# Optimization experiments

Measured on AMD Instinct MI355X. Metric: run time of the kernel, lower is better.

## Reference

```python
import jax, jax.numpy as jnp
import numpy as np

N_E = 1024
E_DIM = 64
BETA = 0.25


def setup_inputs() -> dict:
    key = jax.random.key(0)
    k_z, k_c = jax.random.split(key)
    z = jax.random.normal(k_z, (64, E_DIM, 32, 32), dtype=jnp.float32)  # [B, e_dim, H, W]
    # Codebook initialized uniform(-1/n_e, 1/n_e) as in the torch module
    codebook = jax.random.uniform(k_c, (N_E, E_DIM), dtype=jnp.float32,
                                  minval=-1.0 / N_E, maxval=1.0 / N_E)
    return {"z": z, "codebook": codebook}


def reference(z, codebook):
    beta = BETA
    n_e, e_dim = codebook.shape
    # [B, e_dim, H, W] -> [B, H, W, e_dim]
    z_nhwc = jnp.transpose(z, (0, 2, 3, 1))
    zf = z_nhwc.reshape(-1, e_dim)  # [N, e_dim]
    # Squared Euclidean distances: ||z||^2 + ||e||^2 - 2 z.e  -> [N, n_e]
    d = (jnp.sum(zf * zf, axis=1, keepdims=True)
         + jnp.sum(codebook * codebook, axis=1)
         - 2.0 * jnp.matmul(zf, codebook.T))
    min_encoding_indices = jnp.argmin(d, axis=1)[:, None]  # [N, 1]
    min_encodings = jax.nn.one_hot(min_encoding_indices[:, 0], n_e, dtype=zf.dtype)  # [N, n_e]
    # Gather codebook rows via one-hot matmul (same math as torch version)
    z_q = jnp.matmul(min_encodings, codebook).reshape(z_nhwc.shape)  # [B,H,W,e_dim]
    sg = jax.lax.stop_gradient
    loss = (jnp.mean((sg(z_nhwc) - z_q) ** 2)
            + beta * jnp.mean((z_nhwc - sg(z_q)) ** 2))
    # Straight-through estimator
    z_q = z_nhwc + sg(z_q - z_nhwc)
    z_q = jnp.transpose(z_q, (0, 3, 1, 2))  # back to [B, e_dim, H, W]
    return (loss, z_q, min_encodings, min_encoding_indices)
```

## Files before the change

### kernel.cpp

```cpp
#include <hip/hip_runtime.h>

#define N_ROWS 65536
#define NE 1024
#define ED 64
#define ERR_GAP 8e-5f

static const size_t OFF_ZQ = 1;
static const size_t OFF_ME = 1 + 4194304;
static const size_t OFF_IDX = OFF_ME + (size_t)N_ROWS * NE;
#define ME_FLOATS ((size_t)N_ROWS * NE)

#define SC_CBF  0
#define SC_Z2   65536
#define SC_FLAG 131072

typedef __attribute__((ext_vector_type(8))) short short8v;
typedef __attribute__((ext_vector_type(4))) float f32x4;

__device__ __forceinline__ unsigned bf16_rne(float v) {
  unsigned u = __float_as_uint(v);
  return (u + 0x7FFFu + ((u >> 16) & 1u)) >> 16;
}

__device__ __forceinline__ void gld16(const void* g, void* l) {
  __builtin_amdgcn_global_load_lds(
      (const __attribute__((address_space(1))) void*)g,
      (__attribute__((address_space(3))) void*)l, 16, 0, 0);
}

__global__ __launch_bounds__(256) void k_fill(float* __restrict__ me) {
  const size_t n4 = (ME_FLOATS - 3) >> 2;
  float4* __restrict__ p4 = reinterpret_cast<float4*>(me + 3);
  const size_t stride = (size_t)gridDim.x * blockDim.x;
  const float4 zero4 = make_float4(0.f, 0.f, 0.f, 0.f);
  for (size_t i = blockIdx.x * (size_t)blockDim.x + threadIdx.x; i < n4; i += stride)
    p4[i] = zero4;
  if (blockIdx.x == 0 && threadIdx.x == 0) {
    me[0] = 0.f; me[1] = 0.f; me[2] = 0.f;
    me[ME_FLOATS - 1] = 0.f;
  }
}

__global__ __launch_bounds__(256) void k_e2cb(const float* __restrict__ cb,
                                              float* __restrict__ e2,
                                              short* __restrict__ cbfrag) {
  const int tid = blockIdx.x * 256 + threadIdx.x;
  const int ct = tid >> 6, lane = tid & 63;
  const int col = ct * 16 + (lane & 15);
  const int k0 = (lane >> 4) * 8;
  const float* __restrict__ ep = cb + (size_t)col * ED + k0;
  short* __restrict__ o = cbfrag + (size_t)ct * 2048 + lane * 8;
  #pragma unroll
  for (int ks = 0; ks < 2; ++ks) {
    short h[8], lo[8];
    #pragma unroll
    for (int i = 0; i < 8; ++i) {
      const float v = ep[ks * 32 + i];
      const unsigned hb = bf16_rne(v);
      const float res = v - __uint_as_float(hb << 16);
      h[i] = (short)hb; lo[i] = (short)bf16_rne(res);
    }
    *(short8v*)(o + (size_t)(0 * 2 + ks) * 512) = *(short8v*)h;
    *(short8v*)(o + (size_t)(1 * 2 + ks) * 512) = *(short8v*)lo;
  }
  if (threadIdx.x < 64) {
    const int j = blockIdx.x * 64 + threadIdx.x;
    const float* __restrict__ e = cb + (size_t)j * ED;
    float r[8];
    #pragma unroll
    for (int i = 0; i < 8; ++i) {
      float v = e[i]; float q = v * v;
      asm volatile("" : "+v"(q)); r[i] = q;
    }
    #pragma unroll
    for (int k = 1; k < 8; ++k)
      #pragma unroll
      for (int i = 0; i < 8; ++i) {
        float v = e[8 * k + i]; float q = v * v;
        asm volatile("" : "+v"(q)); r[i] += q;
      }
    e2[j] = ((r[0] + r[1]) + (r[2] + r[3])) + ((r[4] + r[5]) + (r[6] + r[7]));
  }
}

__global__ __launch_bounds__(256, 4) void k_dist(const float* __restrict__ z,
    const short* __restrict__ cbfrag, const float* __restrict__ e2g,
    float* __restrict__ z2g, float* __restrict__ idxf, int* __restrict__ flag) {
  __shared__ float4 smem4[2320];
  short* lBs = (short*)smem4;
  float* e2l = (float*)(smem4 + 2048);
  float* z2l = (float*)(smem4 + 2304);
  float (*lzf)[65] = (float(*)[65])smem4;

  const int t = threadIdx.x, w = t >> 6, lane = t & 63;
  const int row0 = blockIdx.x * 64;

  gld16(e2g + w * 256 + lane * 4, e2l + w * 256);

  const int rl = w * 16 + (lane & 15);
  const int n0 = row0 + rl;
  const int bb = n0 >> 10, hw = n0 & 1023;
  const float* __restrict__ zp = z + (size_t)bb * 65536 + hw;
  const int k0 = (lane >> 4) * 8;
  #pragma unroll
  for (int ks = 0; ks < 2; ++ks)
    #pragma unroll
    for (int i = 0; i < 8; ++i)
      lzf[ks * 32 + k0 + i][rl] = zp[(size_t)(ks * 32 + k0 + i) << 10];
  __syncthreads();

  short8v a[2][2];
  #pragma unroll
  for (int ks = 0; ks < 2; ++ks) {
    short h[8], lo[8];
    #pragma unroll
    for (int i = 0; i < 8; ++i) {
      const float v = lzf[ks * 32 + k0 + i][rl];
      const unsigned hb = bf16_rne(v);
      const float res = v - __uint_as_float(hb << 16);
      h[i] = (short)hb; lo[i] = (short)bf16_rne(res);
    }
    a[0][ks] = *(short8v*)h;
    a[1][ks] = *(short8v*)lo;
  }
  if (t < 64) {
    float r[8];
    #pragma unroll
    for (int i = 0; i < 8; ++i) {
      const float v = lzf[i][t];
      float q = v * v; asm volatile("" : "+v"(q)); r[i] = q;
    }
    #pragma unroll
    for (int k = 1; k < 8; ++k)
      #pragma unroll
      for (int i = 0; i < 8; ++i) {
        const float v = lzf[8 * k + i][t];
        float q = v * v; asm volatile("" : "+v"(q)); r[i] += q;
      }
    const float z2v = ((r[0] + r[1]) + (r[2] + r[3])) + ((r[4] + r[5]) + (r[6] + r[7]));
    z2g[row0 + t] = z2v;
    z2l[t] = z2v;
  }
  __syncthreads();

  #pragma unroll
  for (int i = 0; i < 4; ++i) {
    const int s = w * 4 + i;
    gld16(cbfrag + s * 512 + lane * 8, lBs + s * 512);
  }
  float z2r[4];
  #pragma unroll
  for (int reg = 0; reg < 4; ++reg)
    z2r[reg] = z2l[w * 16 + (lane >> 4) * 4 + reg];
  float Tm[4], Ts[4]; int Tb[4];
  #pragma unroll
  for (int reg = 0; reg < 4; ++reg) { Tm[reg] = 1e30f; Ts[reg] = 1e30f; Tb[reg] = 0; }
  __syncthreads();

  int buf = 0;
  for (int c = 0; c < 16; ++c) {
    if (c < 15) {
      #pragma unroll
      for (int i = 0; i < 4; ++i) {
        const int s = w * 4 + i;
        gld16(cbfrag + (size_t)(c + 1) * 8192 + s * 512 + lane * 8,
              lBs + (buf ^ 1) * 8192 + s * 512);
      }
    }
    #pragma unroll 1
    for (int ctl = 0; ctl < 4; ++ctl) {
      short8v bfr[2][2];
      #pragma unroll
      for (int hl = 0; hl < 2; ++hl)
        #pragma unroll
        for (int ks = 0; ks < 2; ++ks)
          bfr[hl][ks] = *(const short8v*)(lBs + buf * 8192 +
              (ctl * 4 + hl * 2 + ks) * 512 + lane * 8);

      f32x4 acc = (f32x4)(0.0f);
      #pragma unroll
      for (int p = 0; p < 3; ++p) {
        const int pa = (p == 2) ? 1 : 0;
        const int pb = (p == 1) ? 1 : 0;
        #pragma unroll
        for (int ks = 0; ks < 2; ++ks)
          acc = __builtin_amdgcn_mfma_f32_16x16x32_bf16(a[pa][ks], bfr[pb][ks], acc, 0, 0, 0);
      }
      const int j = c * 64 + ctl * 16 + (lane & 15);
      const float e2v = e2l[j];
      #pragma unroll
      for (int reg = 0; reg < 4; ++reg) {
        const float dd = (z2r[reg] + e2v) - 2.0f * acc[reg];
        if (dd < Tm[reg]) { Ts[reg] = Tm[reg]; Tm[reg] = dd; Tb[reg] = j; }
        else { Ts[reg] = fminf(Ts[reg], dd); }
      }
    }
    __syncthreads();
    buf ^= 1;
  }

  #pragma unroll
  for (int reg = 0; reg < 4; ++reg) {
    float m = Tm[reg], s = Ts[reg]; int bi = Tb[reg];
    #pragma unroll
    for (int off = 1; off < 16; off <<= 1) {
      const float om = __shfl_xor(m, off, 64);
      const float os = __shfl_xor(s, off, 64);
      const int   oi = __shfl_xor(bi, off, 64);
      if (om < m || (om == m && oi < bi)) { s = fminf(m, os); m = om; bi = oi; }
      else { s = fminf(s, om); }
    }
    if ((lane & 15) == 0) {
      const int n = row0 + w * 16 + (lane >> 4) * 4 + reg;
      idxf[n] = (float)bi;
      flag[n] = (s - m < ERR_GAP) ? 1 : 0;
    }
  }
}

__global__ __launch_bounds__(256) void k_exact2(const float* __restrict__ z,
    const float* __restrict__ cb, const float* __restrict__ e2,
    const float* __restrict__ z2g, const int* __restrict__ flag,
    float* __restrict__ idxf) {
  __shared__ float zrow[64];
  __shared__ unsigned long long maskS;
  __shared__ float redM[4];
  __shared__ int   redI[4];
  const int t = threadIdx.x, w = t >> 6, lane = t & 63;
  const int row0 = blockIdx.x * 64;
  if (t < 64) {
    const unsigned long long mk = __ballot(flag[row0 + lane] != 0);
    if (lane == 0) maskS = mk;
  }
  __syncthreads();
  unsigned long long mask = maskS;
  while (mask) {
    const int bit = __ffsll((long long)mask) - 1; mask &= mask - 1;
    const int n = row0 + bit;
    const int b = n >> 10, hw = n & 1023;
    if (t < 64) zrow[t] = z[(size_t)b * 65536 + ((size_t)t << 10) + hw];
    __syncthreads();
    const float z2v = z2g[n];
    const float* __restrict__ e0 = cb + (size_t)t * 256;
    float a0 = 0.f, a1 = 0.f, a2 = 0.f, a3 = 0.f;
    #pragma unroll
    for (int k = 0; k < 64; ++k) {
      const float zk = zrow[k];
      a0 = fmaf(zk, e0[k],       a0);
      a1 = fmaf(zk, e0[64 + k],  a1);
      a2 = fmaf(zk, e0[128 + k], a2);
      a3 = fmaf(zk, e0[192 + k], a3);
    }
    float bm = 1e30f; int bi = 0;
    const float d0 = (z2v + e2[t * 4 + 0]) - 2.0f * a0;
    const float d1 = (z2v + e2[t * 4 + 1]) - 2.0f * a1;
    const float d2 = (z2v + e2[t * 4 + 2]) - 2.0f * a2;
    const float d3 = (z2v + e2[t * 4 + 3]) - 2.0f * a3;
    if (d0 < bm) { bm = d0; bi = t * 4 + 0; }
    if (d1 < bm) { bm = d1; bi = t * 4 + 1; }
    if (d2 < bm) { bm = d2; bi = t * 4 + 2; }
    if (d3 < bm) { bm = d3; bi = t * 4 + 3; }
    #pragma unroll
    for (int off = 1; off < 64; off <<= 1) {
      const float om = __shfl_xor(bm, off, 64);
      const int   oi = __shfl_xor(bi, off, 64);
      if (om < bm || (om == bm && oi < bi)) { bm = om; bi = oi; }
    }
    if (lane == 0) { redM[w] = bm; redI[w] = bi; }
    __syncthreads();
    if (t == 0) {
      float m = redM[0]; int i0 = redI[0];
      #pragma unroll
      for (int ww = 1; ww < 4; ++ww) {
        if (redM[ww] < m || (redM[ww] == m && redI[ww] < i0)) { m = redM[ww]; i0 = redI[ww]; }
      }
      idxf[n] = (float)i0;
    }
    __syncthreads();
  }
}

__global__ __launch_bounds__(256) void k_zq(const float* __restrict__ z,
    const float* __restrict__ cb, const float* __restrict__ idxf,
    float* __restrict__ zq, float* __restrict__ partial, float* __restrict__ me) {
  float s = 0.f;
  #pragma unroll 1
  for (int it = 0; it < 8; ++it) {
    const int o = (it * 2048 + blockIdx.x) * 256 + threadIdx.x;
    const int b = o >> 16;
    const int d = (o >> 10) & 63;
    const int hw = o & 1023;
    const int n = (b << 10) + hw;
    const int idx = (int)idxf[n];
    const float v = cb[(size_t)idx * ED + d];
    zq[o] = v;
    if (d == 0) me[(size_t)n * NE + idx] = 1.0f;
    const float diff = z[o] - v;
    s = fmaf(diff, diff, s);
  }
  #pragma unroll
  for (int off = 32; off > 0; off >>= 1) s += __shfl_xor(s, off, 64);
  __shared__ float sh[4];
  if ((threadIdx.x & 63) == 0) sh[threadIdx.x >> 6] = s;
  __syncthreads();
  if (threadIdx.x == 0)
    partial[blockIdx.x] = (sh[0] + sh[1]) + (sh[2] + sh[3]);
}

__global__ void k_loss(const float* __restrict__ partial, float* __restrict__ out0) {
  const int t = threadIdx.x;
  double s = 0.0;
  #pragma unroll
  for (int k = 0; k < 8; ++k) s += (double)partial[t + (k << 8)];
  #pragma unroll
  for (int off = 32; off > 0; off >>= 1) s += __shfl_xor(s, off, 64);
  __shared__ double sh[4];
  if ((t & 63) == 0) sh[t >> 6] = s;
  __syncthreads();
  if (t == 0)
    out0[0] = (float)(1.25 * ((sh[0] + sh[1]) + (sh[2] + sh[3])) / 4194304.0);
}

extern "C" void kernel_launch(void* const* d_in, const int* in_sizes, int n_in,
                              void* d_out, int out_size, void* d_ws, size_t ws_size,
                              hipStream_t stream) {
  const float* z  = (const float*)d_in[0];
  const float* cb = (const float*)d_in[1];
  float* out  = (float*)d_out;
  float* zq   = out + OFF_ZQ;
  float* me   = out + OFF_ME;
  float* idxf = out + OFF_IDX;
  float* sbase = out + 4;
  short* cbfrag = (short*)(sbase + SC_CBF);
  float* z2     = sbase + SC_Z2;
  int*   flag   = (int*)(sbase + SC_FLAG);
  float* e2      = (float*)((char*)d_ws + 16);
  float* partial = (float*)((char*)d_ws + 4112);

  k_fill<<<2048, 256, 0, stream>>>(me);
  k_e2cb<<<16, 256, 0, stream>>>(cb, e2, cbfrag);
  k_dist<<<1024, 256, 0, stream>>>(z, cbfrag, e2, z2, idxf, flag);
  k_exact2<<<1024, 256, 0, stream>>>(z, cb, e2, z2, flag, idxf);
  k_zq<<<2048, 256, 0, stream>>>(z, cb, idxf, zq, partial, me);
  k_loss<<<1, 256, 0, stream>>>(partial, out);
}
```

Measured before the change: 198.1 us.

## Batch flagged rows per block in exact rescoring, keep codebook rows in registers

The exact fp32 recheck kernel now stages every flagged row of the 64-row tile in shared memory up front, then walks the codebook in four groups of 256 entries. Each thread holds one codebook row in registers and scores it against all flagged rows. Before, each flagged row was handled serially and re-streamed the whole codebook from global memory. The aim is to reuse the codebook across flagged rows and to return early from blocks with no flagged rows. The cost is two block-wide barriers per row per group and a 64-float4 register footprint that may limit occupancy.

```diff
diff --git a/kernel.cpp b/kernel.cpp
--- a/kernel.cpp
+++ b/kernel.cpp
@@ -218,66 +218,85 @@
   }
 }
 
-__global__ __launch_bounds__(256) void k_exact2(const float* __restrict__ z,
-    const float* __restrict__ cb, const float* __restrict__ e2,
+__global__ __launch_bounds__(256, 2) void k_exact3(const float* __restrict__ z,
+    const float* __restrict__ cb, const float* __restrict__ e2g,
     const float* __restrict__ z2g, const int* __restrict__ flag,
     float* __restrict__ idxf) {
-  __shared__ float zrow[64];
+  __shared__ float zAll[64][64];
+  __shared__ float z2All[64];
+  __shared__ int   rowIdx[64];
+  __shared__ float bestM[64];
+  __shared__ int   bestI[64];
+  __shared__ float wredM[4];
+  __shared__ int   wredI[4];
   __shared__ unsigned long long maskS;
-  __shared__ float redM[4];
-  __shared__ int   redI[4];
   const int t = threadIdx.x, w = t >> 6, lane = t & 63;
   const int row0 = blockIdx.x * 64;
+
   if (t < 64) {
     const unsigned long long mk = __ballot(flag[row0 + lane] != 0);
     if (lane == 0) maskS = mk;
   }
   __syncthreads();
-  unsigned long long mask = maskS;
-  while (mask) {
-    const int bit = __ffsll((long long)mask) - 1; mask &= mask - 1;
-    const int n = row0 + bit;
+  const unsigned long long mask0 = maskS;
+  if (mask0 == 0) return;
+  const int nrows = __popcll(mask0);
+
+  if (t < 64 && (mask0 >> t) & 1ull) {
+    const int rank = __popcll(mask0 & ((1ull << t) - 1ull));
+    rowIdx[rank] = row0 + t;
+  }
+  __syncthreads();
+  for (int i = w; i < nrows; i += 4) {
+    const int n = rowIdx[i];
     const int b = n >> 10, hw = n & 1023;
-    if (t < 64) zrow[t] = z[(size_t)b * 65536 + ((size_t)t << 10) + hw];
-    __syncthreads();
-    const float z2v = z2g[n];
-    const float* __restrict__ e0 = cb + (size_t)t * 256;
-    float a0 = 0.f, a1 = 0.f, a2 = 0.f, a3 = 0.f;
-    #pragma unroll
-    for (int k = 0; k < 64; ++k) {
-      const float zk = zrow[k];
-      a0 = fmaf(zk, e0[k],       a0);
-      a1 = fmaf(zk, e0[64 + k],  a1);
-      a2 = fmaf(zk, e0[128 + k], a2);
-      a3 = fmaf(zk, e0[192 + k], a3);
-    }
-    float bm = 1e30f; int bi = 0;
-    const float d0 = (z2v + e2[t * 4 + 0]) - 2.0f * a0;
-    const float d1 = (z2v + e2[t * 4 + 1]) - 2.0f * a1;
-    const float d2 = (z2v + e2[t * 4 + 2]) - 2.0f * a2;
-    const float d3 = (z2v + e2[t * 4 + 3]) - 2.0f * a3;
-    if (d0 < bm) { bm = d0; bi = t * 4 + 0; }
-    if (d1 < bm) { bm = d1; bi = t * 4 + 1; }
-    if (d2 < bm) { bm = d2; bi = t * 4 + 2; }
-    if (d3 < bm) { bm = d3; bi = t * 4 + 3; }
-    #pragma unroll
-    for (int off = 1; off < 64; off <<= 1) {
-      const float om = __shfl_xor(bm, off, 64);
-      const int   oi = __shfl_xor(bi, off, 64);
-      if (om < bm || (om == bm && oi < bi)) { bm = om; bi = oi; }
-    }
-    if (lane == 0) { redM[w] = bm; redI[w] = bi; }
-    __syncthreads();
-    if (t == 0) {
-      float m = redM[0]; int i0 = redI[0];
-      #pragma unroll
-      for (int ww = 1; ww < 4; ++ww) {
-        if (redM[ww] < m || (redM[ww] == m && redI[ww] < i0)) { m = redM[ww]; i0 = redI[ww]; }
-      }
-      idxf[n] = (float)i0;
-    }
-    __syncthreads();
-  }
+    zAll[i][lane] = z[(size_t)b * 65536 + ((size_t)lane << 10) + hw];
+    if (lane == 0) z2All[i] = z2g[n];
+  }
+  if (t < 64) { bestM[t] = 1e30f; bestI[t] = 0; }
+  __syncthreads();
+
+  #pragma unroll 1
+  for (int g = 0; g < 4; ++g) {
+    const int j = g * 256 + t;
+    float4 er4[16];
+    const float4* __restrict__ cbp = (const float4*)(cb + (size_t)j * ED);
+    #pragma unroll
+    for (int q = 0; q < 16; ++q) er4[q] = cbp[q];
+    const float e2v = e2g[j];
+    #pragma unroll 1
+    for (int i = 0; i < nrows; ++i) {
+      float a = 0.f;
+      #pragma unroll
+      for (int q = 0; q < 16; ++q) {
+        a = fmaf(zAll[i][4 * q + 0], er4[q].x, a);
+        a = fmaf(zAll[i][4 * q + 1], er4[q].y, a);
+        a = fmaf(zAll[i][4 * q + 2], er4[q].z, a);
+        a = fmaf(zAll[i][4 * q + 3], er4[q].w, a);
+      }
+      float d = (z2All[i] + e2v) - 2.0f * a;
+      int bi = j;
+      #pragma unroll
+      for (int off = 1; off < 64; off <<= 1) {
+        const float om = __shfl_xor(d, off, 64);
+        const int   oi = __shfl_xor(bi, off, 64);
+        if (om < d || (om == d && oi < bi)) { d = om; bi = oi; }
+      }
+      if (lane == 0) { wredM[w] = d; wredI[w] = bi; }
+      __syncthreads();
+      if (t == 0) {
+        float m = bestM[i]; int mi = bestI[i];
+        #pragma unroll
+        for (int ww = 0; ww < 4; ++ww)
+          if (wredM[ww] < m || (wredM[ww] == m && wredI[ww] < mi)) {
+            m = wredM[ww]; mi = wredI[ww];
+          }
+        bestM[i] = m; bestI[i] = mi;
+      }
+      __syncthreads();
+    }
+  }
+  if (t < nrows) idxf[rowIdx[t]] = (float)bestI[t];
 }
 
 __global__ __launch_bounds__(256) void k_zq(const float* __restrict__ z,
@@ -340,7 +359,7 @@
   k_fill<<<2048, 256, 0, stream>>>(me);
   k_e2cb<<<16, 256, 0, stream>>>(cb, e2, cbfrag);
   k_dist<<<1024, 256, 0, stream>>>(z, cbfrag, e2, z2, idxf, flag);
-  k_exact2<<<1024, 256, 0, stream>>>(z, cb, e2, z2, flag, idxf);
+  k_exact3<<<1024, 256, 0, stream>>>(z, cb, e2, z2, flag, idxf);
   k_zq<<<2048, 256, 0, stream>>>(z, cb, idxf, zq, partial, me);
   k_loss<<<1, 256, 0, stream>>>(partial, out);
 }
```

Measured after the change: 190.4 us. 1.04x faster.
